# Optimization experiments

Measured on AMD Instinct MI355X. Metric: run time of the kernel, lower is better.

## Reference

```python
import jax, jax.numpy as jnp
import numpy as np

C = 128
HID = 4 * C
K = 7
PAD = K // 2
B, T, F = 4, 512, 128
LN_EPS = 1e-5
LS_INIT = 1e-2  # LayerScale init value


def setup_inputs() -> dict:
    key = jax.random.key(0)
    ks = jax.random.split(key, 4)
    x = jax.random.normal(ks[0], (B, C, T, F), dtype=jnp.float32)
    dw_w = jax.random.normal(ks[1], (C, 1, K, K), dtype=jnp.float32) * (1.0 / K)
    dw_b = jnp.zeros((C,), dtype=jnp.float32)
    ln_g = jnp.ones((C,), dtype=jnp.float32)
    ln_b = jnp.zeros((C,), dtype=jnp.float32)
    w1 = jax.random.normal(ks[2], (HID, C), dtype=jnp.float32) * (1.0 / np.sqrt(C))
    b1 = jnp.zeros((HID,), dtype=jnp.float32)
    w2 = jax.random.normal(ks[3], (C, HID), dtype=jnp.float32) * (1.0 / np.sqrt(HID))
    b2 = jnp.zeros((C,), dtype=jnp.float32)
    ls = jnp.full((C,), LS_INIT, dtype=jnp.float32)
    return {"x": x, "dw_w": dw_w, "dw_b": dw_b, "ln_g": ln_g, "ln_b": ln_b,
            "w1": w1, "b1": b1, "w2": w2, "b2": b2, "ls": ls}


def reference(x, dw_w, dw_b, ln_g, ln_b, w1, b1, w2, b2, ls):
    # depthwise 2D conv over (T, F), groups = C
    y = jax.lax.conv_general_dilated(
        x, dw_w, window_strides=(1, 1), padding=[(PAD, PAD), (PAD, PAD)],
        feature_group_count=x.shape[1],
        dimension_numbers=("NCHW", "OIHW", "NCHW"))
    y = y + dw_b[None, :, None, None]
    # channels-last for LayerNorm over C and pointwise MLP
    y = jnp.transpose(y, (0, 2, 3, 1))  # [B, T, F, C]
    mu = jnp.mean(y, axis=-1, keepdims=True)
    var = jnp.mean(jnp.square(y - mu), axis=-1, keepdims=True)
    y = (y - mu) * jax.lax.rsqrt(var + LN_EPS) * ln_g + ln_b
    # pointwise MLP: C -> 4C -> GELU -> C
    h = jax.nn.gelu(jnp.einsum("btfc,hc->btfh", y, w1) + b1)
    y = jnp.einsum("btfh,ch->btfc", h, w2) + b2
    # LayerScale: per-channel multiply
    y = y * ls
    return jnp.transpose(y, (0, 3, 1, 2))  # back to [B, C, T, F]
```

## Files before the change

kernel.cpp:

```cpp
#include <hip/hip_runtime.h>
#include <hip/hip_bf16.h>
#include <math.h>

typedef __bf16 bf16x8 __attribute__((ext_vector_type(8)));
typedef float f32x4 __attribute__((ext_vector_type(4)));

constexpr int C_ = 128, HID_ = 512, T_ = 512, F_ = 128, B_ = 4;
constexpr int PIMG = T_ * F_;

__global__ void wcvt_k(const float* __restrict__ w1, const float* __restrict__ w2,
                       __bf16* __restrict__ w1b, __bf16* __restrict__ w2b) {
    int i = blockIdx.x * 256 + threadIdx.x;
    w1b[i] = (__bf16)w1[i];
    w2b[i] = (__bf16)w2[i];
}

template <typename OT>
__global__ __launch_bounds__(256) void dwconv_k(
    const float* __restrict__ x, const float* __restrict__ dww,
    const float* __restrict__ dwb, OT* __restrict__ y) {
    __shared__ float tile[38][140];
    const int bx = blockIdx.x;
    const int tt = bx & 15, c = (bx >> 4) & 127, b = bx >> 11;
    const int t0 = tt * 32;
    const float* xp = x + ((size_t)(b * C_ + c)) * PIMG;

    float wr[49];
#pragma unroll
    for (int i = 0; i < 49; ++i) wr[i] = dww[c * 49 + i];
    const float bias = dwb[c];

    const int colq = threadIdx.x & 31;
    const int rg = threadIdx.x >> 5;
    for (int r = rg; r < 38; r += 8) {
        const int t = t0 - 3 + r;
        f32x4 v = {0.f, 0.f, 0.f, 0.f};
        if (t >= 0 && t < T_) v = *(const f32x4*)(xp + (size_t)t * F_ + colq * 4);
        *(f32x4*)&tile[r][4 + colq * 4] = v;
        if (colq == 0) { tile[r][1] = 0.f; tile[r][2] = 0.f; tile[r][3] = 0.f; }
        if (colq == 31) { tile[r][132] = 0.f; tile[r][133] = 0.f; tile[r][134] = 0.f; }
    }
    __syncthreads();

    const int f = threadIdx.x & 127;
    const int g = threadIdx.x >> 7;
    float acc[16];
#pragma unroll
    for (int i = 0; i < 16; ++i) acc[i] = 0.f;
#pragma unroll
    for (int df = 0; df < 7; ++df) {
        float colv[22];
#pragma unroll
        for (int j = 0; j < 22; ++j) colv[j] = tile[g * 16 + j][1 + f + df];
#pragma unroll
        for (int dr = 0; dr < 7; ++dr) {
            const float wv = wr[dr * 7 + df];
#pragma unroll
            for (int i = 0; i < 16; ++i) acc[i] += colv[i + dr] * wv;
        }
    }
    OT* yp = y + ((size_t)(b * C_ + c)) * PIMG + (size_t)(t0 + g * 16) * F_ + f;
#pragma unroll
    for (int i = 0; i < 16; ++i) yp[(size_t)i * F_] = (OT)(acc[i] + bias);
}

__device__ __forceinline__ float gelu_tanh(float xv) {
    const float u2 = 1.5957691216057308f * (xv + 0.044715f * xv * xv * xv);
    const float e = __expf(-u2);
    return __fdividef(xv, 1.f + e);
}

template <typename YT>
__global__ __launch_bounds__(512, 4) void lnmlp_k(
    const YT* y,
    const __bf16* __restrict__ w1b, const __bf16* __restrict__ w2b,
    const float* __restrict__ lng, const float* __restrict__ lnb,
    const float* __restrict__ b1, const float* __restrict__ b2,
    const float* __restrict__ ls, float* out) {
    constexpr bool YBF = (sizeof(YT) == 2);
    constexpr int YRAW_BYTES = YBF ? 16384 : 34816;
    constexpr int SMEM_SZ = YRAW_BYTES + 17408;
    __shared__ __align__(16) unsigned char smem[SMEM_SZ];
    unsigned short (*yraw_b)[64] = (unsigned short (*)[64])smem;
    float (*yraw_f)[68] = (float (*)[68])smem;
    unsigned short (*yb)[136] = (unsigned short (*)[136])(smem + YRAW_BYTES);
    unsigned short (*hl)[264] = (unsigned short (*)[264])smem;
    __shared__ double pls[8][64], pls2[8][64];
    __shared__ double mud[64], rsd[64];
    __shared__ float lgs[C_], lbs[C_];

    const int tid = threadIdx.x;
    const int lane = tid & 63, wv = tid >> 6;
    const int b = blockIdx.x >> 10;
    const int p0 = (blockIdx.x & 1023) * 64;
    const YT* yp = y + (size_t)b * ((size_t)C_ * PIMG) + p0;

    if (tid < 128) lgs[tid] = lng[tid];
    else if (tid < 256) lbs[tid - 128] = lnb[tid - 128];

    if constexpr (YBF) {
#pragma unroll
        for (int it = 0; it < 2; ++it) {
            const int row0 = it * 64 + wv * 8;
            const YT* gsrc = yp + (size_t)(row0 + (lane >> 3)) * PIMG + (lane & 7) * 8;
            __builtin_amdgcn_global_load_lds((const unsigned int*)gsrc,
                                             (unsigned int*)&yraw_b[row0][0], 16, 0, 0);
        }
    } else {
#pragma unroll
        for (int it = 0; it < 4; ++it) {
            const int c = it * 32 + (tid >> 4);
            const int ch = (tid & 15) * 4;
            *(f32x4*)&yraw_f[c][ch] = *(const f32x4*)(yp + (size_t)c * PIMG + ch);
        }
    }
    __syncthreads();

    auto ldy = [&](int c, int p) -> float {
        if constexpr (YBF) return (float)__builtin_bit_cast(__bf16, yraw_b[c][p]);
        else return yraw_f[c][p];
    };

    {
        double s = 0.0, s2 = 0.0;
#pragma unroll
        for (int i = 0; i < 16; ++i) {
            const double v = (double)ldy(wv * 16 + i, lane);
            s += v;
            s2 = fma(v, v, s2);
        }
        pls[wv][lane] = s;
        pls2[wv][lane] = s2;
    }
    __syncthreads();

    if (tid < 64) {
        const int p = tid;
        double s = 0.0, s2 = 0.0;
#pragma unroll
        for (int w = 0; w < 8; ++w) { s += pls[w][p]; s2 += pls2[w][p]; }
        const double mu = s * (1.0 / 128.0);
        const double var = (s2 - s * s * (1.0 / 128.0)) * (1.0 / 128.0);
        mud[p] = mu;
        rsd[p] = 1.0 / sqrt(var + 1e-5);
    }
    __syncthreads();

    {
        const int pos = tid & 63;
        const int cbase = (tid >> 6) * 16;
        const double mu = mud[pos], rs = rsd[pos];
#pragma unroll
        for (int j = 0; j < 16; j += 2) {
            const int c = cbase + j;
            const float v0 = (float)(((double)ldy(c, pos) - mu) * rs) * lgs[c] + lbs[c];
            const float v1 = (float)(((double)ldy(c + 1, pos) - mu) * rs) * lgs[c + 1] + lbs[c + 1];
            *(unsigned int*)&yb[pos][c] =
                (unsigned int)__builtin_bit_cast(unsigned short, (__bf16)v0) |
                ((unsigned int)__builtin_bit_cast(unsigned short, (__bf16)v1) << 16);
        }
    }
    __syncthreads();

    const int l15 = lane & 15, l4 = lane >> 4;

    f32x4 acc1[4][4];
#pragma unroll
    for (int m = 0; m < 4; ++m)
#pragma unroll
        for (int ct = 0; ct < 4; ++ct) acc1[m][ct] = (f32x4){0.f, 0.f, 0.f, 0.f};

    const __bf16* w1p = w1b + (size_t)(wv * 64) * 128;
#pragma unroll
    for (int k0 = 0; k0 < 128; k0 += 32) {
        bf16x8 bh[4];
#pragma unroll
        for (int ct = 0; ct < 4; ++ct)
            bh[ct] = *(const bf16x8*)&yb[ct * 16 + l15][k0 + l4 * 8];
#pragma unroll
        for (int m = 0; m < 4; ++m) {
            bf16x8 ah = *(const bf16x8*)(w1p + (size_t)(m * 16 + l15) * 128 + k0 + l4 * 8);
#pragma unroll
            for (int ct = 0; ct < 4; ++ct)
                acc1[m][ct] = __builtin_amdgcn_mfma_f32_16x16x32_bf16(ah, bh[ct], acc1[m][ct], 0, 0, 0);
        }
    }
    __syncthreads();

    auto gelu_store = [&]() {
#pragma unroll
        for (int m = 0; m < 4; ++m) {
            const int hid0 = wv * 64 + m * 16 + l4 * 4;
            const int col0 = (wv & 3) * 64 + m * 16 + l4 * 4;
            const float bb0 = b1[hid0], bb1 = b1[hid0 + 1];
            const float bb2v = b1[hid0 + 2], bb3 = b1[hid0 + 3];
#pragma unroll
            for (int ct = 0; ct < 4; ++ct) {
                const int p = ct * 16 + l15;
                float hv[4];
                hv[0] = gelu_tanh(acc1[m][ct][0] + bb0);
                hv[1] = gelu_tanh(acc1[m][ct][1] + bb1);
                hv[2] = gelu_tanh(acc1[m][ct][2] + bb2v);
                hv[3] = gelu_tanh(acc1[m][ct][3] + bb3);
                unsigned int lo = (unsigned int)__builtin_bit_cast(unsigned short, (__bf16)hv[0]) |
                                  ((unsigned int)__builtin_bit_cast(unsigned short, (__bf16)hv[1]) << 16);
                unsigned int hi = (unsigned int)__builtin_bit_cast(unsigned short, (__bf16)hv[2]) |
                                  ((unsigned int)__builtin_bit_cast(unsigned short, (__bf16)hv[3]) << 16);
                *(unsigned long long*)&hl[p][col0] =
                    (unsigned long long)lo | ((unsigned long long)hi << 32);
            }
        }
    };

    if (wv < 4) gelu_store();
    __syncthreads();

    f32x4 acc2[4];
#pragma unroll
    for (int ct = 0; ct < 4; ++ct) acc2[ct] = (f32x4){0.f, 0.f, 0.f, 0.f};
    const __bf16* w2p = w2b + (size_t)(wv * 16) * 512;

#pragma unroll
    for (int k0 = 0; k0 < 256; k0 += 32) {
        bf16x8 bh[4];
#pragma unroll
        for (int ct = 0; ct < 4; ++ct)
            bh[ct] = *(const bf16x8*)&hl[ct * 16 + l15][k0 + l4 * 8];
        bf16x8 ah = *(const bf16x8*)(w2p + (size_t)l15 * 512 + k0 + l4 * 8);
#pragma unroll
        for (int ct = 0; ct < 4; ++ct)
            acc2[ct] = __builtin_amdgcn_mfma_f32_16x16x32_bf16(ah, bh[ct], acc2[ct], 0, 0, 0);
    }
    __syncthreads();

    if (wv >= 4) gelu_store();
    __syncthreads();

#pragma unroll
    for (int k0 = 256; k0 < 512; k0 += 32) {
        bf16x8 bh[4];
#pragma unroll
        for (int ct = 0; ct < 4; ++ct)
            bh[ct] = *(const bf16x8*)&hl[ct * 16 + l15][(k0 - 256) + l4 * 8];
        bf16x8 ah = *(const bf16x8*)(w2p + (size_t)l15 * 512 + k0 + l4 * 8);
#pragma unroll
        for (int ct = 0; ct < 4; ++ct)
            acc2[ct] = __builtin_amdgcn_mfma_f32_16x16x32_bf16(ah, bh[ct], acc2[ct], 0, 0, 0);
    }

    float* op = out + (size_t)b * ((size_t)C_ * PIMG) + p0;
    {
        const int c0 = wv * 16 + l4 * 4;
        float bv[4], lv[4];
#pragma unroll
        for (int r = 0; r < 4; ++r) { bv[r] = b2[c0 + r]; lv[r] = ls[c0 + r]; }
#pragma unroll
        for (int ct = 0; ct < 4; ++ct) {
            const int p = ct * 16 + l15;
#pragma unroll
            for (int r = 0; r < 4; ++r)
                op[(size_t)(c0 + r) * PIMG + p] = (acc2[ct][r] + bv[r]) * lv[r];
        }
    }
}

extern "C" void kernel_launch(void* const* d_in, const int* in_sizes, int n_in,
                              void* d_out, int out_size, void* d_ws, size_t ws_size,
                              hipStream_t stream) {
    const float* x   = (const float*)d_in[0];
    const float* dww = (const float*)d_in[1];
    const float* dwb = (const float*)d_in[2];
    const float* lng = (const float*)d_in[3];
    const float* lnb = (const float*)d_in[4];
    const float* w1  = (const float*)d_in[5];
    const float* b1  = (const float*)d_in[6];
    const float* w2  = (const float*)d_in[7];
    const float* b2  = (const float*)d_in[8];
    const float* ls  = (const float*)d_in[9];
    float* out = (float*)d_out;

    __bf16* w1b = (__bf16*)d_ws;
    __bf16* w2b = w1b + 65536;
    wcvt_k<<<65536 / 256, 256, 0, stream>>>(w1, w2, w1b, w2b);

    const size_t interElems = (size_t)B_ * C_ * PIMG;
    const size_t needWs = 262144 + interElems * 2;
    if (ws_size >= needWs) {
        __bf16* yc = (__bf16*)((char*)d_ws + 262144);
        dwconv_k<__bf16><<<B_ * C_ * (T_ / 32), 256, 0, stream>>>(x, dww, dwb, yc);
        lnmlp_k<__bf16><<<B_ * (PIMG / 64), 512, 0, stream>>>(yc, w1b, w2b,
                                                              lng, lnb, b1, b2, ls, out);
    } else {
        float* yc = out;
        dwconv_k<float><<<B_ * C_ * (T_ / 32), 256, 0, stream>>>(x, dww, dwb, yc);
        lnmlp_k<float><<<B_ * (PIMG / 64), 512, 0, stream>>>(yc, w1b, w2b,
                                                             lng, lnb, b1, b2, ls, out);
    }
}
```

Measured before the change: 256.6 us.

## Split GEMM1 into two half-width passes and shrink LN partial-sum storage

The first MLP GEMM now runs as two passes, each producing 256 hidden units, with all 8 waves sharing each half. Before, each wave computed 64 hidden units at once and half the waves waited to store them. This halves the acc1 register footprint and removes the idle-wave imbalance in the GELU store, at the cost of reading the LN output tile from LDS twice. LayerNorm partial sums now accumulate in float rather than double, and the shared-memory buffers are re-laid out into one aliased arena. The normalized-output store is also widened to 64-bit writes.

Result: no change. 253.6 us (-1.2%).

```diff
diff --git a/kernel.cpp b/kernel.cpp
--- a/kernel.cpp
+++ b/kernel.cpp
@@ -78,16 +78,23 @@
     const float* __restrict__ b1, const float* __restrict__ b2,
     const float* __restrict__ ls, float* out) {
     constexpr bool YBF = (sizeof(YT) == 2);
+    constexpr int YB_BYTES = 17408;
     constexpr int YRAW_BYTES = YBF ? 16384 : 34816;
-    constexpr int SMEM_SZ = YRAW_BYTES + 17408;
+    constexpr int FRESH_OFF = YB_BYTES + YRAW_BYTES;
+    constexpr int CHUNK_END = YB_BYTES + 33792;
+    constexpr int A_ = FRESH_OFF + 6144;
+    constexpr int SMEM_SZ = (A_ > CHUNK_END) ? A_ : CHUNK_END;
     __shared__ __align__(16) unsigned char smem[SMEM_SZ];
-    unsigned short (*yraw_b)[64] = (unsigned short (*)[64])smem;
-    float (*yraw_f)[68] = (float (*)[68])smem;
-    unsigned short (*yb)[136] = (unsigned short (*)[136])(smem + YRAW_BYTES);
-    unsigned short (*hl)[264] = (unsigned short (*)[264])smem;
-    __shared__ double pls[8][64], pls2[8][64];
-    __shared__ double mud[64], rsd[64];
-    __shared__ float lgs[C_], lbs[C_];
+    unsigned short (*yb)[136] = (unsigned short (*)[136])smem;
+    unsigned short (*yraw_b)[64] = (unsigned short (*)[64])(smem + YB_BYTES);
+    float (*yraw_f)[68] = (float (*)[68])(smem + YB_BYTES);
+    unsigned short (*hl)[264] = (unsigned short (*)[264])(smem + YB_BYTES);
+    float (*pls)[64] = (float (*)[64])(smem + FRESH_OFF);
+    float (*pls2)[64] = (float (*)[64])(smem + FRESH_OFF + 2048);
+    double* mud = (double*)(smem + FRESH_OFF + 4096);
+    double* rsd = (double*)(smem + FRESH_OFF + 4608);
+    float* lgs = (float*)(smem + FRESH_OFF + 5120);
+    float* lbs = (float*)(smem + FRESH_OFF + 5632);
 
     const int tid = threadIdx.x;
     const int lane = tid & 63, wv = tid >> 6;
@@ -122,12 +129,12 @@
     };
 
     {
-        double s = 0.0, s2 = 0.0;
+        float s = 0.f, s2 = 0.f;
 #pragma unroll
         for (int i = 0; i < 16; ++i) {
-            const double v = (double)ldy(wv * 16 + i, lane);
+            const float v = ldy(wv * 16 + i, lane);
             s += v;
-            s2 = fma(v, v, s2);
+            s2 = fmaf(v, v, s2);
         }
         pls[wv][lane] = s;
         pls2[wv][lane] = s2;
@@ -138,7 +145,7 @@
         const int p = tid;
         double s = 0.0, s2 = 0.0;
 #pragma unroll
-        for (int w = 0; w < 8; ++w) { s += pls[w][p]; s2 += pls2[w][p]; }
+        for (int w = 0; w < 8; ++w) { s += (double)pls[w][p]; s2 += (double)pls2[w][p]; }
         const double mu = s * (1.0 / 128.0);
         const double var = (s2 - s * s * (1.0 / 128.0)) * (1.0 / 128.0);
         mud[p] = mu;
@@ -151,47 +158,53 @@
         const int cbase = (tid >> 6) * 16;
         const double mu = mud[pos], rs = rsd[pos];
 #pragma unroll
-        for (int j = 0; j < 16; j += 2) {
+        for (int j = 0; j < 16; j += 4) {
             const int c = cbase + j;
-            const float v0 = (float)(((double)ldy(c, pos) - mu) * rs) * lgs[c] + lbs[c];
-            const float v1 = (float)(((double)ldy(c + 1, pos) - mu) * rs) * lgs[c + 1] + lbs[c + 1];
-            *(unsigned int*)&yb[pos][c] =
-                (unsigned int)__builtin_bit_cast(unsigned short, (__bf16)v0) |
-                ((unsigned int)__builtin_bit_cast(unsigned short, (__bf16)v1) << 16);
+            unsigned int pk[2];
+#pragma unroll
+            for (int q = 0; q < 2; ++q) {
+                const int cc = c + 2 * q;
+                const float v0 = (float)(((double)ldy(cc, pos) - mu) * rs) * lgs[cc] + lbs[cc];
+                const float v1 = (float)(((double)ldy(cc + 1, pos) - mu) * rs) * lgs[cc + 1] + lbs[cc + 1];
+                pk[q] = (unsigned int)__builtin_bit_cast(unsigned short, (__bf16)v0) |
+                        ((unsigned int)__builtin_bit_cast(unsigned short, (__bf16)v1) << 16);
+            }
+            *(unsigned long long*)&yb[pos][c] =
+                (unsigned long long)pk[0] | ((unsigned long long)pk[1] << 32);
         }
     }
     __syncthreads();
 
     const int l15 = lane & 15, l4 = lane >> 4;
 
-    f32x4 acc1[4][4];
-#pragma unroll
-    for (int m = 0; m < 4; ++m)
-#pragma unroll
-        for (int ct = 0; ct < 4; ++ct) acc1[m][ct] = (f32x4){0.f, 0.f, 0.f, 0.f};
-
-    const __bf16* w1p = w1b + (size_t)(wv * 64) * 128;
-#pragma unroll
-    for (int k0 = 0; k0 < 128; k0 += 32) {
-        bf16x8 bh[4];
-#pragma unroll
-        for (int ct = 0; ct < 4; ++ct)
-            bh[ct] = *(const bf16x8*)&yb[ct * 16 + l15][k0 + l4 * 8];
-#pragma unroll
-        for (int m = 0; m < 4; ++m) {
-            bf16x8 ah = *(const bf16x8*)(w1p + (size_t)(m * 16 + l15) * 128 + k0 + l4 * 8);
+    f32x4 acc1[2][4];
+    auto gemm1_pass = [&](int hbase) {
+#pragma unroll
+        for (int m = 0; m < 2; ++m)
+#pragma unroll
+            for (int ct = 0; ct < 4; ++ct) acc1[m][ct] = (f32x4){0.f, 0.f, 0.f, 0.f};
+        const __bf16* w1p = w1b + (size_t)hbase * 128;
+#pragma unroll
+        for (int k0 = 0; k0 < 128; k0 += 32) {
+            bf16x8 bh[4];
 #pragma unroll
             for (int ct = 0; ct < 4; ++ct)
-                acc1[m][ct] = __builtin_amdgcn_mfma_f32_16x16x32_bf16(ah, bh[ct], acc1[m][ct], 0, 0, 0);
-        }
-    }
-    __syncthreads();
-
-    auto gelu_store = [&]() {
-#pragma unroll
-        for (int m = 0; m < 4; ++m) {
-            const int hid0 = wv * 64 + m * 16 + l4 * 4;
-            const int col0 = (wv & 3) * 64 + m * 16 + l4 * 4;
+                bh[ct] = *(const bf16x8*)&yb[ct * 16 + l15][k0 + l4 * 8];
+#pragma unroll
+            for (int m = 0; m < 2; ++m) {
+                bf16x8 ah = *(const bf16x8*)(w1p + (size_t)(m * 16 + l15) * 128 + k0 + l4 * 8);
+#pragma unroll
+                for (int ct = 0; ct < 4; ++ct)
+                    acc1[m][ct] = __builtin_amdgcn_mfma_f32_16x16x32_bf16(ah, bh[ct], acc1[m][ct], 0, 0, 0);
+            }
+        }
+    };
+
+    auto gelu_store = [&](int hbase, int cbase2) {
+#pragma unroll
+        for (int m = 0; m < 2; ++m) {
+            const int hid0 = hbase + m * 16 + l4 * 4;
+            const int col0 = cbase2 + m * 16 + l4 * 4;
             const float bb0 = b1[hid0], bb1 = b1[hid0 + 1];
             const float bb2v = b1[hid0 + 2], bb3 = b1[hid0 + 3];
 #pragma unroll
@@ -212,7 +225,8 @@
         }
     };
 
-    if (wv < 4) gelu_store();
+    gemm1_pass(wv * 32);
+    gelu_store(wv * 32, wv * 32);
     __syncthreads();
 
     f32x4 acc2[4];
@@ -233,7 +247,8 @@
     }
     __syncthreads();
 
-    if (wv >= 4) gelu_store();
+    gemm1_pass(256 + wv * 32);
+    gelu_store(256 + wv * 32, wv * 32);
     __syncthreads();
 
 #pragma unroll
```
